# Performance work log

Measured on AMD Instinct MI355X. Metric: run time of the kernel, lower is better.

## Reference

```python
import jax, jax.numpy as jnp
import numpy as np

STOCH, DETER, HID, OBS, ACT = 32, 512, 512, 18, 4
MIN_STD, EPS, UPD_BIAS = 0.1, 1e-3, -1.0


def _ln(x, g, b):
    m = x.mean(-1, keepdims=True)
    v = ((x - m) ** 2).mean(-1, keepdims=True)
    return (x - m) * jax.lax.rsqrt(v + EPS) * g + b


def setup_inputs() -> dict:
    key = jax.random.key(0)
    ks = jax.random.split(key, 10)
    B, T = 256, 256
    def w(k, i, o):
        return jax.random.normal(k, (i, o), jnp.float32) / np.float32(np.sqrt(i))
    return {
        "obs": jax.random.normal(ks[0], (B, T, OBS), jnp.float32),
        "action": jax.random.normal(ks[1], (B, T, ACT), jnp.float32),
        "is_first": jax.random.randint(ks[2], (B, T), 0, 2, jnp.int32),
        "w_prior_in": w(ks[3], STOCH + ACT, HID),
        "g_prior_in": jnp.ones(HID, jnp.float32),
        "bb_prior_in": jnp.zeros(HID, jnp.float32),
        "w_gru": w(ks[4], HID + DETER, 3 * DETER),
        "g_gru": jnp.ones(3 * DETER, jnp.float32),
        "bb_gru": jnp.zeros(3 * DETER, jnp.float32),
        "w_prior_out": w(ks[5], DETER, HID),
        "g_prior_out": jnp.ones(HID, jnp.float32),
        "bb_prior_out": jnp.zeros(HID, jnp.float32),
        "w_prior_stats": w(ks[6], HID, 2 * STOCH),
        "b_prior_stats": jnp.zeros(2 * STOCH, jnp.float32),
        "w_post": w(ks[7], DETER + OBS, HID),
        "g_post": jnp.ones(HID, jnp.float32),
        "bb_post": jnp.zeros(HID, jnp.float32),
        "w_post_stats": w(ks[8], HID, 2 * STOCH),
        "b_post_stats": jnp.zeros(2 * STOCH, jnp.float32),
        "initial_deter": 0.1 * jax.random.normal(ks[9], (1, DETER), jnp.float32),
    }


def reference(obs, action, is_first,
              w_prior_in, g_prior_in, bb_prior_in,
              w_gru, g_gru, bb_gru,
              w_prior_out, g_prior_out, bb_prior_out,
              w_prior_stats, b_prior_stats,
              w_post, g_post, bb_post,
              w_post_stats, b_post_stats,
              initial_deter):
    """RSSM.observe with sample=False. Returns (B, T, 2*(DETER+3*STOCH)):
    concat of post[deter,stoch,mean,std] and prior[deter,stoch,mean,std];
    stoch == mean since dist.mean is used."""
    B = obs.shape[0]
    # learned initial state (identical for every batch row / reset)
    deter0 = jnp.tanh(initial_deter)                                  # (1, DETER)
    h0 = jax.nn.silu(_ln(deter0 @ w_prior_out, g_prior_out, bb_prior_out))
    s0 = h0 @ w_prior_stats + b_prior_stats
    init_mean, _ = jnp.split(s0, 2, axis=-1)                          # (1, STOCH)

    def step(carry, xs):
        deter, stoch = carry
        o_t, a_t, f_t = xs
        mask = (f_t > 0)[:, None]
        deter = jnp.where(mask, deter0, deter)
        stoch = jnp.where(mask, init_mean, stoch)
        a_t = jnp.where(mask, 0.0, a_t)
        # prior_in
        h = jax.nn.silu(_ln(jnp.concatenate([stoch, a_t], -1) @ w_prior_in,
                            g_prior_in, bb_prior_in))
        # GRU cell (depth=1)
        gates = _ln(jnp.concatenate([h, deter], -1) @ w_gru, g_gru, bb_gru)
        r, c, u = jnp.split(gates, 3, axis=-1)
        r = jax.nn.sigmoid(r)
        u = jax.nn.sigmoid(u + UPD_BIAS)
        cand = jax.nn.silu(r * c)
        deter = u * cand + (1.0 - u) * deter
        # prior stats
        h2 = jax.nn.silu(_ln(deter @ w_prior_out, g_prior_out, bb_prior_out))
        ps = h2 @ w_prior_stats + b_prior_stats
        pm, psd = jnp.split(ps, 2, axis=-1)
        psd = jax.nn.softplus(psd) + MIN_STD
        # posterior
        h3 = jax.nn.silu(_ln(jnp.concatenate([deter, o_t], -1) @ w_post,
                             g_post, bb_post))
        qs = h3 @ w_post_stats + b_post_stats
        qm, qsd = jnp.split(qs, 2, axis=-1)
        qsd = jax.nn.softplus(qsd) + MIN_STD
        out = jnp.concatenate([deter, qm, qm, qsd, deter, pm, pm, psd], -1)
        return (deter, qm), out

    carry0 = (jnp.broadcast_to(deter0, (B, DETER)),
              jnp.broadcast_to(init_mean, (B, STOCH)))
    xs = (obs.swapaxes(0, 1), action.swapaxes(0, 1), is_first.swapaxes(0, 1))
    _, ys = jax.lax.scan(step, carry0, xs)   # (T, B, 2*(DETER+3*STOCH))
    return ys.swapaxes(0, 1)
```

## Files before the change

### kernel.cpp

```cpp
#include <hip/hip_runtime.h>

#define TT 256
#define BDIM 256
#define MT 32

typedef unsigned short u16;
typedef unsigned int u32;
typedef __attribute__((ext_vector_type(8))) short bf16x8;
typedef __attribute__((ext_vector_type(4))) float f32x4;

#define GLL(g, l) __builtin_amdgcn_global_load_lds( \
    (const __attribute__((address_space(1))) void*)(g), \
    (__attribute__((address_space(3))) void*)(l), 16, 0, 0)

struct P {
  const float* obs; const float* action; const int* is_first;
  const float* w_prior_in; const float* g_prior_in; const float* bb_prior_in;
  const float* w_gru; const float* g_gru; const float* bb_gru;
  const float* w_prior_out; const float* g_prior_out; const float* bb_prior_out;
  const float* w_prior_stats; const float* b_prior_stats;
  const float* w_post; const float* g_post; const float* bb_post;
  const float* w_post_stats; const float* b_post_stats;
  const float* initial_deter;
  float* out;
  u16 *WgT3;
  u16 *W2T3;
  u16 *WsT3;
  float *deter0, *init_mean;
  int *segb, *segt0, *nact;
  u16 *arow;
  u16 *h2;
  float *gates;
  float *hraw;
  float *deter;
  float *stoch;
  int NB;
};

__device__ __forceinline__ float b2f(u16 u) {
  union { float f; u32 i; } v; v.i = ((u32)u) << 16; return v.f;
}
__device__ __forceinline__ u16 f2b(float f) {
  union { float f; u32 i; } v; v.f = f;
  u32 r = v.i + 0x7FFF + ((v.i >> 16) & 1);
  return (u16)(r >> 16);
}
__device__ __forceinline__ float sigm(float x) { return 1.f / (1.f + __expf(-x)); }
__device__ __forceinline__ float splus(float x) { return x > 15.f ? x : log1pf(__expf(x)); }

__device__ __forceinline__ void awr2(u16* base, int i, int kk, u16 hi, u16 lo) {
  size_t o = (size_t)(kk >> 5) << 11;
  int sw = ((i << 5) + (kk & 31)) ^ ((i & 7) << 3);
  base[o + sw] = hi;
  base[o + 1024 + sw] = lo;
}

__device__ __forceinline__ void h_from_x(const P& p, u16* slotA, int i, float xv, int lane) {
  float a0[8];
  #pragma unroll
  for (int c = 0; c < 8; ++c) a0[c] = 0.f;
  #pragma unroll 4
  for (int j = 0; j < 36; ++j) {
    float s = __shfl(xv, j, 64);
    const float* wr = p.w_prior_in + j * 512 + lane;
    #pragma unroll
    for (int c = 0; c < 8; ++c) a0[c] = fmaf(s, wr[c << 6], a0[c]);
  }
  float sm = 0.f, sq = 0.f;
  #pragma unroll
  for (int c = 0; c < 8; ++c) { sm += a0[c]; sq += a0[c] * a0[c]; }
  #pragma unroll
  for (int o = 32; o; o >>= 1) { sm += __shfl_xor(sm, o); sq += __shfl_xor(sq, o); }
  float m = sm * (1.f / 512.f);
  float rs = rsqrtf(sq * (1.f / 512.f) - m * m + 1e-3f);
  #pragma unroll
  for (int c = 0; c < 8; ++c) {
    int col = lane + (c << 6);
    float v = (a0[c] - m) * rs * p.g_prior_in[col] + p.bb_prior_in[col];
    v = v * sigm(v);
    u16 hi = f2b(v);
    awr2(slotA, i, 544 + col, hi, f2b(v - b2f(hi)));
  }
}

__global__ void k_weights(P p) {
  const int E1 = 192 * 16384, E2 = 68 * 16384, E3 = 32 * 8192;
  const int total = E1 + E2 + E3;
  for (int idx = blockIdx.x * blockDim.x + threadIdx.x; idx < total;
       idx += gridDim.x * blockDim.x) {
    float w; u16* dst;
    int pl;
    if (idx < E1) {
      int kk = idx & 31, prow = (idx >> 5) & 511, img = idx >> 14;
      int pc = img / 6, np = img - pc * 6;
      pl = prow >> 8;
      int n = np * 256 + (prow & 255), k = (pc << 5) + kk;
      w = (k < 512) ? p.w_gru[(512 + k) * 1536 + n] : p.w_gru[(k - 512) * 1536 + n];
      dst = p.WgT3 + ((size_t)img << 14) + (((prow << 5) + kk) ^ ((prow & 7) << 3));
    } else if (idx < E1 + E2) {
      int t = idx - E1;
      int kk = t & 31, prow = (t >> 5) & 511, img = t >> 14;
      int pc = img >> 2, np = img & 3;
      pl = prow >> 8;
      int n = np * 256 + (prow & 255), k = (pc << 5) + kk;
      if (k < 512) w = (n < 512) ? p.w_prior_out[k * 512 + n] : p.w_post[k * 512 + (n - 512)];
      else { int j = k - 512; w = (n >= 512 && j < 18) ? p.w_post[(512 + j) * 512 + (n - 512)] : 0.f; }
      dst = p.W2T3 + ((size_t)img << 14) + (((prow << 5) + kk) ^ ((prow & 7) << 3));
    } else {
      int t = idx - E1 - E2;
      int kk = t & 31, prow = (t >> 5) & 255, pc = t >> 13;
      pl = prow >> 7;
      int nl = prow & 127, k = (pc << 5) + kk;
      if (nl < 64) w = (k < 512) ? p.w_prior_stats[k * 64 + nl] : 0.f;
      else         w = (k >= 512) ? p.w_post_stats[(k - 512) * 64 + (nl - 64)] : 0.f;
      dst = p.WsT3 + ((size_t)pc << 13) + (((prow << 5) + kk) ^ ((prow & 7) << 3));
    }
    u16 hi = f2b(w);
    *dst = pl ? f2b(w - b2f(hi)) : hi;
  }
}

__global__ void k_init_state(P p) {
  __shared__ float d0s[512], tmp[512], red[256];
  int tid = threadIdx.x;
  for (int n = tid; n < 512; n += 256) { d0s[n] = tanhf(p.initial_deter[n]); p.deter0[n] = d0s[n]; }
  __syncthreads();
  for (int n = tid; n < 512; n += 256) {
    float s = 0.f;
    for (int d = 0; d < 512; ++d) s = fmaf(d0s[d], p.w_prior_out[d * 512 + n], s);
    tmp[n] = s;
  }
  __syncthreads();
  float ls = 0.f, lq = 0.f;
  for (int n = tid; n < 512; n += 256) { ls += tmp[n]; lq += tmp[n] * tmp[n]; }
  red[tid] = ls; __syncthreads();
  for (int s = 128; s; s >>= 1) { if (tid < s) red[tid] += red[tid + s]; __syncthreads(); }
  float m = red[0] * (1.f / 512.f); __syncthreads();
  red[tid] = lq; __syncthreads();
  for (int s = 128; s; s >>= 1) { if (tid < s) red[tid] += red[tid + s]; __syncthreads(); }
  float rs = rsqrtf(red[0] * (1.f / 512.f) - m * m + 1e-3f); __syncthreads();
  for (int n = tid; n < 512; n += 256) {
    float h = (tmp[n] - m) * rs * p.g_prior_out[n] + p.bb_prior_out[n];
    tmp[n] = h * sigm(h);
  }
  __syncthreads();
  if (tid < 32) {
    float s = 0.f;
    for (int d = 0; d < 512; ++d) s = fmaf(tmp[d], p.w_prior_stats[d * 64 + tid], s);
    p.init_mean[tid] = s + p.b_prior_stats[tid];
  }
}

__global__ void k_segments(P p) {
  __shared__ int hist[257], off[258], cur[257];
  int tid = threadIdx.x;
  for (int i = tid; i < 257; i += 256) hist[i] = 0;
  __syncthreads();
  int b = tid;
  { int t = 0;
    while (t < TT) {
      int t0 = t; t++;
      while (t < TT && p.is_first[b * TT + t] == 0) t++;
      atomicAdd(&hist[t - t0], 1);
    } }
  __syncthreads();
  if (tid == 0) {
    int run = 0;
    for (int len = 256; len >= 0; --len) { off[len] = run; run += hist[len]; }
  }
  __syncthreads();
  for (int i = tid; i < 257; i += 256) { cur[i] = off[i]; p.nact[i] = off[i]; }
  __syncthreads();
  { int t = 0;
    while (t < TT) {
      int t0 = t; t++;
      while (t < TT && p.is_first[b * TT + t] == 0) t++;
      int idx = atomicAdd(&cur[t - t0], 1);
      p.segb[idx] = b; p.segt0[idx] = t0;
    } }
}

template<int NI, int NSTEPS, int JAT, int RPP>
__device__ __forceinline__ void gemm_pass(
    const u16* __restrict__ aBase, const u16* __restrict__ wBase, int wStride,
    u16* ldsA, u16* ldsW, int wave, int lane, int quad, int l15,
    f32x4 (&acc)[2][NI]) {
  constexpr int GPW = 1 + (RPP >> 5);

  auto stage = [&](int st, int buf) {
    int apc = (st >= JAT) ? st + 1 : st;
    GLL(aBase + ((size_t)apc << 11) + (wave << 9) + (lane << 3),
        ldsA + (buf << 11) + (wave << 9));
    const u16* wS = wBase + (size_t)st * wStride;
    u16* wD = ldsW + (buf << 14);
    #pragma unroll
    for (int pp = 0; pp < 2; ++pp)
      #pragma unroll
      for (int c = 0; c < (RPP >> 6); ++c) {
        int ro = pp * RPP + wave * (RPP >> 2) + (c << 4);
        GLL(wS + (ro << 5) + (lane << 3), wD + (ro << 5));
      }
  };
  auto compute = [&](int buf) {
    const u16* A = ldsA + (buf << 11);
    const u16* W = ldsW + (buf << 14);
    int xr = (l15 & 7) << 3;
    bf16x8 ah[2], al[2];
    #pragma unroll
    for (int mi = 0; mi < 2; ++mi) {
      int r0 = mi * 16 + l15;
      ah[mi] = *(const bf16x8*)&A[((r0 << 5) + (quad << 3)) ^ xr];
      al[mi] = *(const bf16x8*)&A[(((32 + r0) << 5) + (quad << 3)) ^ xr];
    }
    #pragma unroll
    for (int ni = 0; ni < NI; ++ni) {
      int rh = wave * (NI * 16) + ni * 16 + l15;
      bf16x8 wh = *(const bf16x8*)&W[((rh << 5) + (quad << 3)) ^ xr];
      bf16x8 wl = *(const bf16x8*)&W[(((RPP + rh) << 5) + (quad << 3)) ^ xr];
      #pragma unroll
      for (int mi = 0; mi < 2; ++mi) {
        acc[mi][ni] = __builtin_amdgcn_mfma_f32_16x16x32_bf16(ah[mi], wh, acc[mi][ni], 0, 0, 0);
        acc[mi][ni] = __builtin_amdgcn_mfma_f32_16x16x32_bf16(al[mi], wh, acc[mi][ni], 0, 0, 0);
        acc[mi][ni] = __builtin_amdgcn_mfma_f32_16x16x32_bf16(ah[mi], wl, acc[mi][ni], 0, 0, 0);
      }
    }
  };

  stage(0, 0); stage(1, 1); stage(2, 2);
  for (int st = 0; st < NSTEPS; ++st) {
    if (st < NSTEPS - 2)
      asm volatile("s_waitcnt vmcnt(%0)" :: "i"(2 * GPW) : "memory");
    else if (st == NSTEPS - 2)
      asm volatile("s_waitcnt vmcnt(%0)" :: "i"(GPW) : "memory");
    else
      asm volatile("s_waitcnt vmcnt(0)" ::: "memory");
    __builtin_amdgcn_s_barrier();
    __builtin_amdgcn_sched_barrier(0);
    if (st + 3 < NSTEPS) stage(st + 3, (st + 3) & 3);
    compute(st & 3);
  }
}

__global__ void __launch_bounds__(BDIM, 1) k_main(P p) {
  __shared__ u16 lds[73728];
  const int tid = threadIdx.x;
  const int wave = tid >> 6, lane = tid & 63, quad = lane >> 4, l15 = lane & 15;
  u16* ldsA = lds;
  u16* ldsW = lds + 8192;
  const int blk = blockIdx.x;
  u16* slotA = p.arow + (size_t)blk * 67584;
  u16* slotH = p.h2 + (size_t)blk * 65536;
  float* slotG = p.gates + (size_t)blk * 49152;
  float* slotR = p.hraw + (size_t)blk * 32768;
  float* slotD = p.deter + (size_t)blk * 16384;
  float* slotS = p.stoch + (size_t)blk * 1024;
  const int S_total = p.nact[0];
  const int ntiles = (S_total + MT - 1) >> 5;
  const int gmax = (ntiles + 255) & ~255;

  for (int g = blk; g < gmax; g += p.NB) {
    int r = g >> 8, w = g & 255;
    int x = w & 7; if (r & 1) x = 7 - x;
    int t = (r << 8) + (x << 5) + ((w >> 3) & 31);
    if (t >= ntiles) continue;
    int row0 = t << 5;
    int nr0 = S_total - row0; if (nr0 > MT) nr0 = MT;

    for (int k = 0;; ++k) {
      int Mk = p.nact[k] - row0; if (Mk > nr0) Mk = nr0;
      if (Mk <= 0) break;

      for (int i = wave; i < Mk; i += 4) {
        int gi = row0 + i;
        int b = p.segb[gi], t0 = p.segt0[gi];
        float xv = 0.f;
        if (k == 0) {
          #pragma unroll
          for (int c = 0; c < 8; ++c) {
            int d = lane + (c << 6);
            float v = p.deter0[d];
            slotD[i * 512 + d] = v;
            u16 hi = f2b(v);
            awr2(slotA, i, d, hi, f2b(v - b2f(hi)));
          }
          int ff = p.is_first[b * TT + t0];
          if (lane < 32) xv = p.init_mean[lane];
          else if (lane < 36) xv = (ff > 0) ? 0.f : p.action[((size_t)b * TT + t0) * 4 + (lane - 32)];
        } else {
          if (lane < 32) xv = slotS[i * 32 + lane];
          else if (lane < 36) xv = p.action[((size_t)b * TT + t0 + k) * 4 + (lane - 32)];
        }
        h_from_x(p, slotA, i, xv, lane);
      }
      __syncthreads();

      for (int np = 0; np < 6; ++np) {
        __syncthreads();
        f32x4 acc[2][4];
        #pragma unroll
        for (int a = 0; a < 2; ++a)
          #pragma unroll
          for (int bq = 0; bq < 4; ++bq) acc[a][bq] = f32x4{0.f, 0.f, 0.f, 0.f};
        gemm_pass<4, 32, 16, 256>(slotA, p.WgT3 + np * 16384, 98304,
                                  ldsA, ldsW, wave, lane, quad, l15, acc);
        #pragma unroll
        for (int mi = 0; mi < 2; ++mi)
          #pragma unroll
          for (int ni = 0; ni < 4; ++ni)
            #pragma unroll
            for (int rr = 0; rr < 4; ++rr)
              slotG[(mi * 16 + quad * 4 + rr) * 1536 + np * 256 + wave * 64 + ni * 16 + l15]
                  = acc[mi][ni][rr];
      }
      __syncthreads();

      for (int i = wave; i < Mk; i += 4) {
        const float* grow = slotG + i * 1536;
        float g24[24];
        float sm = 0.f, sq = 0.f;
        #pragma unroll
        for (int c = 0; c < 24; ++c) {
          g24[c] = grow[lane + (c << 6)];
          sm += g24[c]; sq += g24[c] * g24[c];
        }
        #pragma unroll
        for (int o = 32; o; o >>= 1) { sm += __shfl_xor(sm, o); sq += __shfl_xor(sq, o); }
        float m = sm * (1.f / 1536.f);
        float rs = rsqrtf(sq * (1.f / 1536.f) - m * m + 1e-3f);
        int gi = row0 + i;
        int b = p.segb[gi], tt = p.segt0[gi] + k;
        float* orow = p.out + ((size_t)b * TT + tt) * 1216;
        #pragma unroll
        for (int c = 0; c < 8; ++c) {
          int d = lane + (c << 6);
          float gr = (g24[c] - m) * rs * p.g_gru[d] + p.bb_gru[d];
          float gc = (g24[c + 8] - m) * rs * p.g_gru[512 + d] + p.bb_gru[512 + d];
          float gu = (g24[c + 16] - m) * rs * p.g_gru[1024 + d] + p.bb_gru[1024 + d];
          float r_ = sigm(gr);
          float u_ = sigm(gu - 1.0f);
          float rc = r_ * gc;
          float cand = rc * sigm(rc);
          float dp = slotD[i * 512 + d];
          float dn = u_ * cand + (1.f - u_) * dp;
          slotD[i * 512 + d] = dn;
          orow[d] = dn; orow[608 + d] = dn;
          u16 hi = f2b(dn);
          awr2(slotA, i, d, hi, f2b(dn - b2f(hi)));
        }
        if (lane < 32) {
          float ov = (lane < 18) ? p.obs[((size_t)b * TT + tt) * 18 + lane] : 0.f;
          u16 hi = f2b(ov);
          awr2(slotA, i, 512 + lane, hi, f2b(ov - b2f(hi)));
        }
      }
      __syncthreads();

      for (int np = 0; np < 4; ++np) {
        __syncthreads();
        f32x4 acc[2][4];
        #pragma unroll
        for (int a = 0; a < 2; ++a)
          #pragma unroll
          for (int bq = 0; bq < 4; ++bq) acc[a][bq] = f32x4{0.f, 0.f, 0.f, 0.f};
        gemm_pass<4, 17, 1000, 256>(slotA, p.W2T3 + np * 16384, 65536,
                                    ldsA, ldsW, wave, lane, quad, l15, acc);
        #pragma unroll
        for (int mi = 0; mi < 2; ++mi)
          #pragma unroll
          for (int ni = 0; ni < 4; ++ni)
            #pragma unroll
            for (int rr = 0; rr < 4; ++rr)
              slotR[(mi * 16 + quad * 4 + rr) * 1024 + np * 256 + wave * 64 + ni * 16 + l15]
                  = acc[mi][ni][rr];
      }
      __syncthreads();

      for (int i = wave; i < Mk; i += 4) {
        #pragma unroll
        for (int hh = 0; hh < 2; ++hh) {
          const float* hb = slotR + i * 1024 + (hh << 9);
          const float* gv = hh ? p.g_post : p.g_prior_out;
          const float* bv = hh ? p.bb_post : p.bb_prior_out;
          float v[8];
          float sm = 0.f, sq = 0.f;
          #pragma unroll
          for (int c = 0; c < 8; ++c) {
            v[c] = hb[lane + (c << 6)];
            sm += v[c]; sq += v[c] * v[c];
          }
          #pragma unroll
          for (int o = 32; o; o >>= 1) { sm += __shfl_xor(sm, o); sq += __shfl_xor(sq, o); }
          float m = sm * (1.f / 512.f);
          float rs = rsqrtf(sq * (1.f / 512.f) - m * m + 1e-3f);
          #pragma unroll
          for (int c = 0; c < 8; ++c) {
            int d = lane + (c << 6);
            float xx = (v[c] - m) * rs * gv[d] + bv[d];
            xx = xx * sigm(xx);
            u16 hi = f2b(xx);
            awr2(slotH, i, (hh << 9) + d, hi, f2b(xx - b2f(hi)));
          }
        }
      }
      __syncthreads();

      {
        f32x4 acc[2][2];
        #pragma unroll
        for (int a = 0; a < 2; ++a)
          #pragma unroll
          for (int bq = 0; bq < 2; ++bq) acc[a][bq] = f32x4{0.f, 0.f, 0.f, 0.f};
        gemm_pass<2, 32, 1000, 128>(slotH, p.WsT3, 8192,
                                    ldsA, ldsW, wave, lane, quad, l15, acc);
        #pragma unroll
        for (int mi = 0; mi < 2; ++mi)
          #pragma unroll
          for (int ni = 0; ni < 2; ++ni)
            #pragma unroll
            for (int rr = 0; rr < 4; ++rr) {
              int i = mi * 16 + quad * 4 + rr;
              int col = wave * 32 + ni * 16 + l15;
              if (i < Mk) {
                float v = acc[mi][ni][rr];
                int gi = row0 + i;
                int b = p.segb[gi], tt = p.segt0[gi] + k;
                float* orow = p.out + ((size_t)b * TT + tt) * 1216;
                if (col < 32) {
                  v += p.b_prior_stats[col];
                  orow[1120 + col] = v; orow[1152 + col] = v;
                } else if (col < 64) {
                  v = splus(v + p.b_prior_stats[col]) + 0.1f;
                  orow[1184 + col - 32] = v;
                } else if (col < 96) {
                  v += p.b_post_stats[col - 64];
                  orow[512 + col - 64] = v; orow[544 + col - 64] = v;
                  slotS[i * 32 + (col - 64)] = v;
                } else {
                  v = splus(v + p.b_post_stats[col - 64]) + 0.1f;
                  orow[576 + col - 96] = v;
                }
              }
            }
      }
      __syncthreads();
    }
  }
}

extern "C" void kernel_launch(void* const* d_in, const int* in_sizes, int n_in,
                              void* d_out, int out_size, void* d_ws, size_t ws_size,
                              hipStream_t stream) {
  P p;
  p.obs = (const float*)d_in[0];
  p.action = (const float*)d_in[1];
  p.is_first = (const int*)d_in[2];
  p.w_prior_in = (const float*)d_in[3];
  p.g_prior_in = (const float*)d_in[4];
  p.bb_prior_in = (const float*)d_in[5];
  p.w_gru = (const float*)d_in[6];
  p.g_gru = (const float*)d_in[7];
  p.bb_gru = (const float*)d_in[8];
  p.w_prior_out = (const float*)d_in[9];
  p.g_prior_out = (const float*)d_in[10];
  p.bb_prior_out = (const float*)d_in[11];
  p.w_prior_stats = (const float*)d_in[12];
  p.b_prior_stats = (const float*)d_in[13];
  p.w_post = (const float*)d_in[14];
  p.g_post = (const float*)d_in[15];
  p.bb_post = (const float*)d_in[16];
  p.w_post_stats = (const float*)d_in[17];
  p.b_post_stats = (const float*)d_in[18];
  p.initial_deter = (const float*)d_in[19];
  p.out = (float*)d_out;

  char* w = (char*)d_ws;
  auto alloc = [&](size_t bytes) -> char* {
    char* r = w; w += (bytes + 255) & ~(size_t)255; return r;
  };
  p.WgT3 = (u16*)alloc((size_t)192 * 16384 * 2);
  p.W2T3 = (u16*)alloc((size_t)68 * 16384 * 2);
  p.WsT3 = (u16*)alloc((size_t)32 * 8192 * 2);
  p.deter0 = (float*)alloc(512 * 4);
  p.init_mean = (float*)alloc(32 * 4);
  p.segb = (int*)alloc((size_t)65536 * 4);
  p.segt0 = (int*)alloc((size_t)65536 * 4);
  p.nact = (int*)alloc(257 * 4);
  size_t used = (size_t)(w - (char*)d_ws);
  size_t avail = ws_size > used ? ws_size - used : 0;
  size_t slot = 666112;
  long long nb = (long long)(avail / slot);
  if (nb > 256) nb = 256;
  if (nb < 1) nb = 1;
  p.NB = (int)nb;
  p.arow = (u16*)alloc((size_t)p.NB * 135168);
  p.h2 = (u16*)alloc((size_t)p.NB * 131072);
  p.gates = (float*)alloc((size_t)p.NB * 196608);
  p.hraw = (float*)alloc((size_t)p.NB * 131072);
  p.deter = (float*)alloc((size_t)p.NB * 65536);
  p.stoch = (float*)alloc((size_t)p.NB * 4096);

  k_weights<<<dim3(256), dim3(256), 0, stream>>>(p);
  k_init_state<<<dim3(1), dim3(256), 0, stream>>>(p);
  k_segments<<<dim3(1), dim3(256), 0, stream>>>(p);
  k_main<<<dim3(p.NB), dim3(BDIM), 0, stream>>>(p);
}
```

Measured before the change: 8.924 ms.

## Keep recurrent state in registers/LDS and stream weights directly into MFMA operands

```diff
diff --git a/kernel.cpp b/kernel.cpp
--- a/kernel.cpp
+++ b/kernel.cpp
@@ -2,7 +2,6 @@
 
 #define TT 256
 #define BDIM 256
-#define MT 32
 
 typedef unsigned short u16;
 typedef unsigned int u32;
@@ -26,14 +25,10 @@
   u16 *WgT3;
   u16 *W2T3;
   u16 *WsT3;
+  float *wpiT;
   float *deter0, *init_mean;
   int *segb, *segt0, *nact;
-  u16 *arow;
   u16 *h2;
-  float *gates;
-  float *hraw;
-  float *deter;
-  float *stoch;
   int NB;
 };
 
@@ -49,22 +44,28 @@
 __device__ __forceinline__ float splus(float x) { return x > 15.f ? x : log1pf(__expf(x)); }
 
 __device__ __forceinline__ void awr2(u16* base, int i, int kk, u16 hi, u16 lo) {
-  size_t o = (size_t)(kk >> 5) << 11;
+  int o = (kk >> 5) << 11;
   int sw = ((i << 5) + (kk & 31)) ^ ((i & 7) << 3);
   base[o + sw] = hi;
   base[o + 1024 + sw] = lo;
 }
 
-__device__ __forceinline__ void h_from_x(const P& p, u16* slotA, int i, float xv, int lane) {
+__device__ __forceinline__ void h_from_x(const P& p, u16* arow, int i, float xv, int lane) {
+  float xs[36];
+  #pragma unroll
+  for (int j = 0; j < 36; ++j) xs[j] = __shfl(xv, j, 64);
   float a0[8];
   #pragma unroll
-  for (int c = 0; c < 8; ++c) a0[c] = 0.f;
-  #pragma unroll 4
-  for (int j = 0; j < 36; ++j) {
-    float s = __shfl(xv, j, 64);
-    const float* wr = p.w_prior_in + j * 512 + lane;
+  for (int c = 0; c < 8; ++c) {
+    const float4* wp = (const float4*)(p.wpiT + (size_t)(lane + (c << 6)) * 36);
+    float s = 0.f;
     #pragma unroll
-    for (int c = 0; c < 8; ++c) a0[c] = fmaf(s, wr[c << 6], a0[c]);
+    for (int t4 = 0; t4 < 9; ++t4) {
+      float4 ww = wp[t4];
+      s = fmaf(xs[4 * t4], ww.x, s); s = fmaf(xs[4 * t4 + 1], ww.y, s);
+      s = fmaf(xs[4 * t4 + 2], ww.z, s); s = fmaf(xs[4 * t4 + 3], ww.w, s);
+    }
+    a0[c] = s;
   }
   float sm = 0.f, sq = 0.f;
   #pragma unroll
@@ -79,44 +80,41 @@
     float v = (a0[c] - m) * rs * p.g_prior_in[col] + p.bb_prior_in[col];
     v = v * sigm(v);
     u16 hi = f2b(v);
-    awr2(slotA, i, 544 + col, hi, f2b(v - b2f(hi)));
+    awr2(arow, i, 544 + col, hi, f2b(v - b2f(hi)));
   }
 }
 
 __global__ void k_weights(P p) {
-  const int E1 = 192 * 16384, E2 = 68 * 16384, E3 = 32 * 8192;
-  const int total = E1 + E2 + E3;
+  const int E1 = 1024 * 1536, E2 = 544 * 1024, E3 = 1024 * 128, E4 = 36 * 512;
+  const int total = E1 + E2 + E3 + E4;
   for (int idx = blockIdx.x * blockDim.x + threadIdx.x; idx < total;
        idx += gridDim.x * blockDim.x) {
-    float w; u16* dst;
-    int pl;
     if (idx < E1) {
-      int kk = idx & 31, prow = (idx >> 5) & 511, img = idx >> 14;
-      int pc = img / 6, np = img - pc * 6;
-      pl = prow >> 8;
-      int n = np * 256 + (prow & 255), k = (pc << 5) + kk;
-      w = (k < 512) ? p.w_gru[(512 + k) * 1536 + n] : p.w_gru[(k - 512) * 1536 + n];
-      dst = p.WgT3 + ((size_t)img << 14) + (((prow << 5) + kk) ^ ((prow & 7) << 3));
+      int k = idx / 1536, n = idx - k * 1536;
+      float w = (k < 512) ? p.w_gru[(512 + k) * 1536 + n] : p.w_gru[(k - 512) * 1536 + n];
+      int np = n >> 8, r = n & 255, pc = k >> 5, kk = k & 31;
+      u16* d = p.WgT3 + ((size_t)(pc * 6 + np) << 14) + (r << 5) + kk;
+      u16 hi = f2b(w); d[0] = hi; d[8192] = f2b(w - b2f(hi));
     } else if (idx < E1 + E2) {
-      int t = idx - E1;
-      int kk = t & 31, prow = (t >> 5) & 511, img = t >> 14;
-      int pc = img >> 2, np = img & 3;
-      pl = prow >> 8;
-      int n = np * 256 + (prow & 255), k = (pc << 5) + kk;
+      int t = idx - E1; int k = t >> 10, n = t & 1023;
+      float w;
       if (k < 512) w = (n < 512) ? p.w_prior_out[k * 512 + n] : p.w_post[k * 512 + (n - 512)];
       else { int j = k - 512; w = (n >= 512 && j < 18) ? p.w_post[(512 + j) * 512 + (n - 512)] : 0.f; }
-      dst = p.W2T3 + ((size_t)img << 14) + (((prow << 5) + kk) ^ ((prow & 7) << 3));
+      int np = n >> 8, r = n & 255, pc = k >> 5, kk = k & 31;
+      u16* d = p.W2T3 + ((size_t)(pc * 4 + np) << 14) + (r << 5) + kk;
+      u16 hi = f2b(w); d[0] = hi; d[8192] = f2b(w - b2f(hi));
+    } else if (idx < E1 + E2 + E3) {
+      int t = idx - E1 - E2; int k = t >> 7, n = t & 127;
+      float w;
+      if (n < 64) w = (k < 512) ? p.w_prior_stats[k * 64 + n] : 0.f;
+      else        w = (k >= 512) ? p.w_post_stats[(k - 512) * 64 + (n - 64)] : 0.f;
+      int pc = k >> 5, kk = k & 31;
+      u16* d = p.WsT3 + ((size_t)pc << 13) + (n << 5) + kk;
+      u16 hi = f2b(w); d[0] = hi; d[4096] = f2b(w - b2f(hi));
     } else {
-      int t = idx - E1 - E2;
-      int kk = t & 31, prow = (t >> 5) & 255, pc = t >> 13;
-      pl = prow >> 7;
-      int nl = prow & 127, k = (pc << 5) + kk;
-      if (nl < 64) w = (k < 512) ? p.w_prior_stats[k * 64 + nl] : 0.f;
-      else         w = (k >= 512) ? p.w_post_stats[(k - 512) * 64 + (nl - 64)] : 0.f;
-      dst = p.WsT3 + ((size_t)pc << 13) + (((prow << 5) + kk) ^ ((prow & 7) << 3));
+      int t = idx - E1 - E2 - E3; int j = t >> 9, col = t & 511;
+      p.wpiT[col * 36 + j] = p.w_prior_in[j * 512 + col];
     }
-    u16 hi = f2b(w);
-    *dst = pl ? f2b(w - b2f(hi)) : hi;
   }
 }
 
@@ -180,96 +178,80 @@
     } }
 }
 
-template<int NI, int NSTEPS, int JAT, int RPP>
-__device__ __forceinline__ void gemm_pass(
-    const u16* __restrict__ aBase, const u16* __restrict__ wBase, int wStride,
-    u16* ldsA, u16* ldsW, int wave, int lane, int quad, int l15,
-    f32x4 (&acc)[2][NI]) {
-  constexpr int GPW = 1 + (RPP >> 5);
-
-  auto stage = [&](int st, int buf) {
-    int apc = (st >= JAT) ? st + 1 : st;
-    GLL(aBase + ((size_t)apc << 11) + (wave << 9) + (lane << 3),
-        ldsA + (buf << 11) + (wave << 9));
-    const u16* wS = wBase + (size_t)st * wStride;
-    u16* wD = ldsW + (buf << 14);
+template<int NSTEPS, int JAT>
+__device__ __forceinline__ void gemm_nb(
+    const u16* aLds, const u16* wImg, size_t wStride,
+    int wave, int quad, int l15, int xr, f32x4 (&acc)[2][4]) {
+  const u16* wq = wImg + ((((wave << 6) + l15) << 5) + (quad << 3));
+  bf16x8 H0[4], L0[4], H1[4], L1[4], H2[4], L2[4];
+  auto ld = [&](bf16x8 (&H)[4], bf16x8 (&L)[4]) {
     #pragma unroll
-    for (int pp = 0; pp < 2; ++pp)
-      #pragma unroll
-      for (int c = 0; c < (RPP >> 6); ++c) {
-        int ro = pp * RPP + wave * (RPP >> 2) + (c << 4);
-        GLL(wS + (ro << 5) + (lane << 3), wD + (ro << 5));
-      }
+    for (int ni = 0; ni < 4; ++ni) {
+      H[ni] = *(const bf16x8*)(wq + (ni << 9));
+      L[ni] = *(const bf16x8*)(wq + 8192 + (ni << 9));
+    }
+    wq += wStride;
   };
-  auto compute = [&](int buf) {
-    const u16* A = ldsA + (buf << 11);
-    const u16* W = ldsW + (buf << 14);
-    int xr = (l15 & 7) << 3;
+  auto cp = [&](int st, bf16x8 (&H)[4], bf16x8 (&L)[4]) {
+    int apc = st + (st >= JAT ? 1 : 0);
+    const u16* A = aLds + (apc << 11);
     bf16x8 ah[2], al[2];
     #pragma unroll
     for (int mi = 0; mi < 2; ++mi) {
-      int r0 = mi * 16 + l15;
-      ah[mi] = *(const bf16x8*)&A[((r0 << 5) + (quad << 3)) ^ xr];
-      al[mi] = *(const bf16x8*)&A[(((32 + r0) << 5) + (quad << 3)) ^ xr];
+      int off = ((((mi << 4) + l15) << 5) + (quad << 3)) ^ xr;
+      ah[mi] = *(const bf16x8*)&A[off];
+      al[mi] = *(const bf16x8*)&A[off + 1024];
     }
     #pragma unroll
-    for (int ni = 0; ni < NI; ++ni) {
-      int rh = wave * (NI * 16) + ni * 16 + l15;
-      bf16x8 wh = *(const bf16x8*)&W[((rh << 5) + (quad << 3)) ^ xr];
-      bf16x8 wl = *(const bf16x8*)&W[(((RPP + rh) << 5) + (quad << 3)) ^ xr];
+    for (int ni = 0; ni < 4; ++ni)
       #pragma unroll
       for (int mi = 0; mi < 2; ++mi) {
-        acc[mi][ni] = __builtin_amdgcn_mfma_f32_16x16x32_bf16(ah[mi], wh, acc[mi][ni], 0, 0, 0);
-        acc[mi][ni] = __builtin_amdgcn_mfma_f32_16x16x32_bf16(al[mi], wh, acc[mi][ni], 0, 0, 0);
-        acc[mi][ni] = __builtin_amdgcn_mfma_f32_16x16x32_bf16(ah[mi], wl, acc[mi][ni], 0, 0, 0);
+        acc[mi][ni] = __builtin_amdgcn_mfma_f32_16x16x32_bf16(ah[mi], H[ni], acc[mi][ni], 0, 0, 0);
+        acc[mi][ni] = __builtin_amdgcn_mfma_f32_16x16x32_bf16(al[mi], H[ni], acc[mi][ni], 0, 0, 0);
+        acc[mi][ni] = __builtin_amdgcn_mfma_f32_16x16x32_bf16(ah[mi], L[ni], acc[mi][ni], 0, 0, 0);
       }
-    }
   };
-
-  stage(0, 0); stage(1, 1); stage(2, 2);
-  for (int st = 0; st < NSTEPS; ++st) {
-    if (st < NSTEPS - 2)
-      asm volatile("s_waitcnt vmcnt(%0)" :: "i"(2 * GPW) : "memory");
-    else if (st == NSTEPS - 2)
-      asm volatile("s_waitcnt vmcnt(%0)" :: "i"(GPW) : "memory");
-    else
-      asm volatile("s_waitcnt vmcnt(0)" ::: "memory");
-    __builtin_amdgcn_s_barrier();
-    __builtin_amdgcn_sched_barrier(0);
-    if (st + 3 < NSTEPS) stage(st + 3, (st + 3) & 3);
-    compute(st & 3);
-  }
+  static_assert(NSTEPS % 3 == 2, "tail assumes NSTEPS==2 mod 3");
+  ld(H0, L0); ld(H1, L1);
+  for (int st = 0; st + 2 < NSTEPS; st += 3) {
+    ld(H2, L2); cp(st, H0, L0);
+    ld(H0, L0); cp(st + 1, H1, L1);
+    ld(H1, L1); cp(st + 2, H2, L2);
+  }
+  cp(NSTEPS - 2, H0, L0);
+  cp(NSTEPS - 1, H1, L1);
 }
 
 __global__ void __launch_bounds__(BDIM, 1) k_main(P p) {
   __shared__ u16 lds[73728];
+  __shared__ float lnscr[4][32][4];
+  __shared__ float stochs[1024];
+  __shared__ int orowt[32];
   const int tid = threadIdx.x;
   const int wave = tid >> 6, lane = tid & 63, quad = lane >> 4, l15 = lane & 15;
-  u16* ldsA = lds;
-  u16* ldsW = lds + 8192;
+  const int xr = (l15 & 7) << 3;
+  u16* arow = lds;
+  u16* fb = lds + 67584;
   const int blk = blockIdx.x;
-  u16* slotA = p.arow + (size_t)blk * 67584;
   u16* slotH = p.h2 + (size_t)blk * 65536;
-  float* slotG = p.gates + (size_t)blk * 49152;
-  float* slotR = p.hraw + (size_t)blk * 32768;
-  float* slotD = p.deter + (size_t)blk * 16384;
-  float* slotS = p.stoch + (size_t)blk * 1024;
   const int S_total = p.nact[0];
-  const int ntiles = (S_total + MT - 1) >> 5;
+  const int ntiles = (S_total + 31) >> 5;
   const int gmax = (ntiles + 255) & ~255;
 
   for (int g = blk; g < gmax; g += p.NB) {
-    int r = g >> 8, w = g & 255;
-    int x = w & 7; if (r & 1) x = 7 - x;
-    int t = (r << 8) + (x << 5) + ((w >> 3) & 31);
+    int rr_ = g >> 8, w = g & 255;
+    int x = w & 7; if (rr_ & 1) x = 7 - x;
+    int t = (rr_ << 8) + (x << 5) + ((w >> 3) & 31);
     if (t >= ntiles) continue;
     int row0 = t << 5;
-    int nr0 = S_total - row0; if (nr0 > MT) nr0 = MT;
+    int nr0 = S_total - row0; if (nr0 > 32) nr0 = 32;
 
     for (int k = 0;; ++k) {
       int Mk = p.nact[k] - row0; if (Mk > nr0) Mk = nr0;
       if (Mk <= 0) break;
 
+      if (tid < 32)
+        orowt[tid] = (tid < Mk) ? (p.segb[row0 + tid] * TT + p.segt0[row0 + tid] + k) : -1;
       for (int i = wave; i < Mk; i += 4) {
         int gi = row0 + i;
         int b = p.segb[gi], t0 = p.segt0[gi];
@@ -279,152 +261,284 @@
           for (int c = 0; c < 8; ++c) {
             int d = lane + (c << 6);
             float v = p.deter0[d];
-            slotD[i * 512 + d] = v;
             u16 hi = f2b(v);
-            awr2(slotA, i, d, hi, f2b(v - b2f(hi)));
+            awr2(arow, i, d, hi, f2b(v - b2f(hi)));
           }
           int ff = p.is_first[b * TT + t0];
           if (lane < 32) xv = p.init_mean[lane];
           else if (lane < 36) xv = (ff > 0) ? 0.f : p.action[((size_t)b * TT + t0) * 4 + (lane - 32)];
         } else {
-          if (lane < 32) xv = slotS[i * 32 + lane];
+          if (lane < 32) xv = stochs[(i << 5) + lane];
           else if (lane < 36) xv = p.action[((size_t)b * TT + t0 + k) * 4 + (lane - 32)];
         }
-        h_from_x(p, slotA, i, xv, lane);
+        int tc = t0 + k;
+        if (lane < 32) {
+          float ov = (lane < 18) ? p.obs[((size_t)b * TT + tc) * 18 + lane] : 0.f;
+          u16 hi = f2b(ov);
+          awr2(arow, i, 512 + lane, hi, f2b(ov - b2f(hi)));
+        }
+        h_from_x(p, arow, i, xv, lane);
       }
       __syncthreads();
 
+      f32x4 acc[6][2][4];
+      #pragma unroll
       for (int np = 0; np < 6; ++np) {
-        __syncthreads();
-        f32x4 acc[2][4];
-        #pragma unroll
-        for (int a = 0; a < 2; ++a)
-          #pragma unroll
-          for (int bq = 0; bq < 4; ++bq) acc[a][bq] = f32x4{0.f, 0.f, 0.f, 0.f};
-        gemm_pass<4, 32, 16, 256>(slotA, p.WgT3 + np * 16384, 98304,
-                                  ldsA, ldsW, wave, lane, quad, l15, acc);
-        #pragma unroll
-        for (int mi = 0; mi < 2; ++mi)
-          #pragma unroll
-          for (int ni = 0; ni < 4; ++ni)
-            #pragma unroll
-            for (int rr = 0; rr < 4; ++rr)
-              slotG[(mi * 16 + quad * 4 + rr) * 1536 + np * 256 + wave * 64 + ni * 16 + l15]
-                  = acc[mi][ni][rr];
+        #pragma unroll
+        for (int mi = 0; mi < 2; ++mi)
+          #pragma unroll
+          for (int ni = 0; ni < 4; ++ni) acc[np][mi][ni] = f32x4{0.f, 0.f, 0.f, 0.f};
+        gemm_nb<32, 16>(arow, p.WgT3 + np * 16384, (size_t)6 * 16384,
+                        wave, quad, l15, xr, acc[np]);
       }
       __syncthreads();
 
-      for (int i = wave; i < Mk; i += 4) {
-        const float* grow = slotG + i * 1536;
-        float g24[24];
-        float sm = 0.f, sq = 0.f;
-        #pragma unroll
-        for (int c = 0; c < 24; ++c) {
-          g24[c] = grow[lane + (c << 6)];
-          sm += g24[c]; sq += g24[c] * g24[c];
+      {
+        float smv[2][4], sqv[2][4];
+        #pragma unroll
+        for (int mi = 0; mi < 2; ++mi)
+          #pragma unroll
+          for (int rg = 0; rg < 4; ++rg) { smv[mi][rg] = 0.f; sqv[mi][rg] = 0.f; }
+        #pragma unroll
+        for (int np = 0; np < 6; ++np)
+          #pragma unroll
+          for (int mi = 0; mi < 2; ++mi)
+            #pragma unroll
+            for (int ni = 0; ni < 4; ++ni)
+              #pragma unroll
+              for (int rg = 0; rg < 4; ++rg) {
+                float v = acc[np][mi][ni][rg];
+                smv[mi][rg] += v; sqv[mi][rg] += v * v;
+              }
+        #pragma unroll
+        for (int mi = 0; mi < 2; ++mi)
+          #pragma unroll
+          for (int rg = 0; rg < 4; ++rg) {
+            float s = smv[mi][rg], qv = sqv[mi][rg];
+            #pragma unroll
+            for (int o = 1; o < 16; o <<= 1) { s += __shfl_xor(s, o); qv += __shfl_xor(qv, o); }
+            smv[mi][rg] = s; sqv[mi][rg] = qv;
+          }
+        if (l15 == 0) {
+          #pragma unroll
+          for (int mi = 0; mi < 2; ++mi)
+            #pragma unroll
+            for (int rg = 0; rg < 4; ++rg) {
+              int row = (mi << 4) + (quad << 2) + rg;
+              lnscr[wave][row][0] = smv[mi][rg];
+              lnscr[wave][row][1] = sqv[mi][rg];
+            }
         }
-        #pragma unroll
-        for (int o = 32; o; o >>= 1) { sm += __shfl_xor(sm, o); sq += __shfl_xor(sq, o); }
-        float m = sm * (1.f / 1536.f);
-        float rs = rsqrtf(sq * (1.f / 1536.f) - m * m + 1e-3f);
-        int gi = row0 + i;
-        int b = p.segb[gi], tt = p.segt0[gi] + k;
-        float* orow = p.out + ((size_t)b * TT + tt) * 1216;
-        #pragma unroll
-        for (int c = 0; c < 8; ++c) {
-          int d = lane + (c << 6);
-          float gr = (g24[c] - m) * rs * p.g_gru[d] + p.bb_gru[d];
-          float gc = (g24[c + 8] - m) * rs * p.g_gru[512 + d] + p.bb_gru[512 + d];
-          float gu = (g24[c + 16] - m) * rs * p.g_gru[1024 + d] + p.bb_gru[1024 + d];
-          float r_ = sigm(gr);
-          float u_ = sigm(gu - 1.0f);
-          float rc = r_ * gc;
-          float cand = rc * sigm(rc);
-          float dp = slotD[i * 512 + d];
-          float dn = u_ * cand + (1.f - u_) * dp;
-          slotD[i * 512 + d] = dn;
-          orow[d] = dn; orow[608 + d] = dn;
-          u16 hi = f2b(dn);
-          awr2(slotA, i, d, hi, f2b(dn - b2f(hi)));
+        __syncthreads();
+        #pragma unroll
+        for (int mi = 0; mi < 2; ++mi)
+          #pragma unroll
+          for (int rg = 0; rg < 4; ++rg) {
+            int row = (mi << 4) + (quad << 2) + rg;
+            float a0 = 0.f, a1 = 0.f;
+            #pragma unroll
+            for (int w2 = 0; w2 < 4; ++w2) {
+              a0 += lnscr[w2][row][0]; a1 += lnscr[w2][row][1];
+            }
+            float m_ = a0 * (1.f / 1536.f);
+            smv[mi][rg] = m_;
+            sqv[mi][rg] = rsqrtf(a1 * (1.f / 1536.f) - m_ * m_ + 1e-3f);
+          }
+        #pragma unroll
+        for (int hh = 0; hh < 2; ++hh)
+          #pragma unroll
+          for (int ni = 0; ni < 4; ++ni) {
+            int dcol = (hh << 8) + (wave << 6) + (ni << 4) + l15;
+            float gR = p.g_gru[dcol], gC = p.g_gru[512 + dcol], gU = p.g_gru[1024 + dcol];
+            float bR = p.bb_gru[dcol], bC = p.bb_gru[512 + dcol], bU = p.bb_gru[1024 + dcol];
+            int pcD = dcol >> 5, kkD = dcol & 31;
+            #pragma unroll
+            for (int mi = 0; mi < 2; ++mi)
+              #pragma unroll
+              for (int rg = 0; rg < 4; ++rg) {
+                int row = (mi << 4) + (quad << 2) + rg;
+                float m_ = smv[mi][rg], rs_ = sqv[mi][rg];
+                float vr = (acc[hh][mi][ni][rg] - m_) * rs_ * gR + bR;
+                float vc = (acc[2 + hh][mi][ni][rg] - m_) * rs_ * gC + bC;
+                float vu = (acc[4 + hh][mi][ni][rg] - m_) * rs_ * gU + bU;
+                float r_ = sigm(vr), u_ = sigm(vu - 1.f);
+                float rc = r_ * vc, cand = rc * sigm(rc);
+                int ab = (pcD << 11) + (((row << 5) + kkD) ^ ((row & 7) << 3));
+                float dp = b2f(arow[ab]) + b2f(arow[ab + 1024]);
+                float dn = u_ * cand + (1.f - u_) * dp;
+                u16 hi = f2b(dn);
+                arow[ab] = hi; arow[ab + 1024] = f2b(dn - b2f(hi));
+                int ot = orowt[row];
+                if (ot >= 0) {
+                  float* orow = p.out + (size_t)ot * 1216;
+                  orow[dcol] = dn; orow[608 + dcol] = dn;
+                }
+              }
+          }
+      }
+      __syncthreads();
+
+      f32x4 dac[4][2][4];
+      #pragma unroll
+      for (int np = 0; np < 4; ++np) {
+        #pragma unroll
+        for (int mi = 0; mi < 2; ++mi)
+          #pragma unroll
+          for (int ni = 0; ni < 4; ++ni) dac[np][mi][ni] = f32x4{0.f, 0.f, 0.f, 0.f};
+        gemm_nb<17, 100>(arow, p.W2T3 + np * 16384, (size_t)4 * 16384,
+                         wave, quad, l15, xr, dac[np]);
+      }
+      {
+        float sP[2][4], qP[2][4], sQ[2][4], qQ[2][4];
+        #pragma unroll
+        for (int mi = 0; mi < 2; ++mi)
+          #pragma unroll
+          for (int rg = 0; rg < 4; ++rg) { sP[mi][rg]=0.f; qP[mi][rg]=0.f; sQ[mi][rg]=0.f; qQ[mi][rg]=0.f; }
+        #pragma unroll
+        for (int np = 0; np < 4; ++np)
+          #pragma unroll
+          for (int mi = 0; mi < 2; ++mi)
+            #pragma unroll
+            for (int ni = 0; ni < 4; ++ni)
+              #pragma unroll
+              for (int rg = 0; rg < 4; ++rg) {
+                float v = dac[np][mi][ni][rg];
+                if (np < 2) { sP[mi][rg] += v; qP[mi][rg] += v * v; }
+                else        { sQ[mi][rg] += v; qQ[mi][rg] += v * v; }
+              }
+        #pragma unroll
+        for (int mi = 0; mi < 2; ++mi)
+          #pragma unroll
+          for (int rg = 0; rg < 4; ++rg) {
+            float a0 = sP[mi][rg], a1 = qP[mi][rg], a2 = sQ[mi][rg], a3 = qQ[mi][rg];
+            #pragma unroll
+            for (int o = 1; o < 16; o <<= 1) {
+              a0 += __shfl_xor(a0, o); a1 += __shfl_xor(a1, o);
+              a2 += __shfl_xor(a2, o); a3 += __shfl_xor(a3, o);
+            }
+            sP[mi][rg] = a0; qP[mi][rg] = a1; sQ[mi][rg] = a2; qQ[mi][rg] = a3;
+          }
+        if (l15 == 0) {
+          #pragma unroll
+          for (int mi = 0; mi < 2; ++mi)
+            #pragma unroll
+            for (int rg = 0; rg < 4; ++rg) {
+              int row = (mi << 4) + (quad << 2) + rg;
+              lnscr[wave][row][0] = sP[mi][rg]; lnscr[wave][row][1] = qP[mi][rg];
+              lnscr[wave][row][2] = sQ[mi][rg]; lnscr[wave][row][3] = qQ[mi][rg];
+            }
         }
-        if (lane < 32) {
-          float ov = (lane < 18) ? p.obs[((size_t)b * TT + tt) * 18 + lane] : 0.f;
-          u16 hi = f2b(ov);
-          awr2(slotA, i, 512 + lane, hi, f2b(ov - b2f(hi)));
+        __syncthreads();
+        float mP[2][4], rP[2][4], mQ[2][4], rQ[2][4];
+        #pragma unroll
+        for (int mi = 0; mi < 2; ++mi)
+          #pragma unroll
+          for (int rg = 0; rg < 4; ++rg) {
+            int row = (mi << 4) + (quad << 2) + rg;
+            float a0 = 0.f, a1 = 0.f, a2 = 0.f, a3 = 0.f;
+            #pragma unroll
+            for (int w2 = 0; w2 < 4; ++w2) {
+              a0 += lnscr[w2][row][0]; a1 += lnscr[w2][row][1];
+              a2 += lnscr[w2][row][2]; a3 += lnscr[w2][row][3];
+            }
+            mP[mi][rg] = a0 * (1.f / 512.f);
+            rP[mi][rg] = rsqrtf(a1 * (1.f / 512.f) - mP[mi][rg] * mP[mi][rg] + 1e-3f);
+            mQ[mi][rg] = a2 * (1.f / 512.f);
+            rQ[mi][rg] = rsqrtf(a3 * (1.f / 512.f) - mQ[mi][rg] * mQ[mi][rg] + 1e-3f);
+          }
+        #pragma unroll
+        for (int np = 0; np < 4; ++np) {
+          const int half = np >> 1;
+          #pragma unroll
+          for (int ni = 0; ni < 4; ++ni) {
+            int col = (np << 8) + (wave << 6) + (ni << 4) + l15;
+            int c5 = col & 511;
+            float gv = half ? p.g_post[c5] : p.g_prior_out[c5];
+            float bv = half ? p.bb_post[c5] : p.bb_prior_out[c5];
+            int pcH = col >> 5, kkH = col & 31;
+            #pragma unroll
+            for (int mi = 0; mi < 2; ++mi)
+              #pragma unroll
+              for (int rg = 0; rg < 4; ++rg) {
+                int row = (mi << 4) + (quad << 2) + rg;
+                float m_ = half ? mQ[mi][rg] : mP[mi][rg];
+                float rs_ = half ? rQ[mi][rg] : rP[mi][rg];
+                float xx = (dac[np][mi][ni][rg] - m_) * rs_ * gv + bv;
+                xx = xx * sigm(xx);
+                u16 hi = f2b(xx);
+                size_t e = ((size_t)pcH << 11) + (((row << 5) + kkH) ^ ((row & 7) << 3));
+                slotH[e] = hi; slotH[e + 1024] = f2b(xx - b2f(hi));
+              }
+          }
         }
       }
       __syncthreads();
 
-      for (int np = 0; np < 4; ++np) {
-        __syncthreads();
-        f32x4 acc[2][4];
-        #pragma unroll
-        for (int a = 0; a < 2; ++a)
-          #pragma unroll
-          for (int bq = 0; bq < 4; ++bq) acc[a][bq] = f32x4{0.f, 0.f, 0.f, 0.f};
-        gemm_pass<4, 17, 1000, 256>(slotA, p.W2T3 + np * 16384, 65536,
-                                    ldsA, ldsW, wave, lane, quad, l15, acc);
-        #pragma unroll
-        for (int mi = 0; mi < 2; ++mi)
-          #pragma unroll
-          for (int ni = 0; ni < 4; ++ni)
-            #pragma unroll
-            for (int rr = 0; rr < 4; ++rr)
-              slotR[(mi * 16 + quad * 4 + rr) * 1024 + np * 256 + wave * 64 + ni * 16 + l15]
-                  = acc[mi][ni][rr];
-      }
-      __syncthreads();
-
-      for (int i = wave; i < Mk; i += 4) {
-        #pragma unroll
-        for (int hh = 0; hh < 2; ++hh) {
-          const float* hb = slotR + i * 1024 + (hh << 9);
-          const float* gv = hh ? p.g_post : p.g_prior_out;
-          const float* bv = hh ? p.bb_post : p.bb_prior_out;
-          float v[8];
-          float sm = 0.f, sq = 0.f;
-          #pragma unroll
-          for (int c = 0; c < 8; ++c) {
-            v[c] = hb[lane + (c << 6)];
-            sm += v[c]; sq += v[c] * v[c];
-          }
-          #pragma unroll
-          for (int o = 32; o; o >>= 1) { sm += __shfl_xor(sm, o); sq += __shfl_xor(sq, o); }
-          float m = sm * (1.f / 512.f);
-          float rs = rsqrtf(sq * (1.f / 512.f) - m * m + 1e-3f);
-          #pragma unroll
-          for (int c = 0; c < 8; ++c) {
-            int d = lane + (c << 6);
-            float xx = (v[c] - m) * rs * gv[d] + bv[d];
-            xx = xx * sigm(xx);
-            u16 hi = f2b(xx);
-            awr2(slotH, i, (hh << 9) + d, hi, f2b(xx - b2f(hi)));
-          }
+      {
+        const u16* wq0 = p.WsT3 + (((wave << 5) + l15) << 5) + (quad << 3);
+        f32x4 fac[2][2];
+        #pragma unroll
+        for (int mi = 0; mi < 2; ++mi)
+          #pragma unroll
+          for (int ni = 0; ni < 2; ++ni) fac[mi][ni] = f32x4{0.f, 0.f, 0.f, 0.f};
+        bf16x8 FH0[2], FL0[2], FH1[2], FL1[2];
+        auto stF = [&](int st, int buf) {
+          GLL(slotH + (st << 11) + (wave << 9) + (lane << 3),
+              fb + (buf << 11) + (wave << 9));
+        };
+        auto ldF = [&](int st, bf16x8 (&FH)[2], bf16x8 (&FL)[2]) {
+          const u16* qq = wq0 + ((size_t)st << 13);
+          #pragma unroll
+          for (int ni = 0; ni < 2; ++ni) {
+            FH[ni] = *(const bf16x8*)(qq + (ni << 9));
+            FL[ni] = *(const bf16x8*)(qq + 4096 + (ni << 9));
+          }
+        };
+        auto cpF = [&](int st, bf16x8 (&FH)[2], bf16x8 (&FL)[2]) {
+          const u16* A = fb + ((st % 3) << 11);
+          bf16x8 ah[2], al[2];
+          #pragma unroll
+          for (int mi = 0; mi < 2; ++mi) {
+            int off = ((((mi << 4) + l15) << 5) + (quad << 3)) ^ xr;
+            ah[mi] = *(const bf16x8*)&A[off];
+            al[mi] = *(const bf16x8*)&A[off + 1024];
+          }
+          #pragma unroll
+          for (int ni = 0; ni < 2; ++ni)
+            #pragma unroll
+            for (int mi = 0; mi < 2; ++mi) {
+              fac[mi][ni] = __builtin_amdgcn_mfma_f32_16x16x32_bf16(ah[mi], FH[ni], fac[mi][ni], 0, 0, 0);
+              fac[mi][ni] = __builtin_amdgcn_mfma_f32_16x16x32_bf16(al[mi], FH[ni], fac[mi][ni], 0, 0, 0);
+              fac[mi][ni] = __builtin_amdgcn_mfma_f32_16x16x32_bf16(ah[mi], FL[ni], fac[mi][ni], 0, 0, 0);
+            }
+        };
+        stF(0, 0); stF(1, 1); ldF(0, FH0, FL0);
+        for (int st = 0; st < 32; st += 2) {
+          asm volatile("s_waitcnt vmcnt(5)" ::: "memory");
+          __builtin_amdgcn_s_barrier();
+          __builtin_amdgcn_sched_barrier(0);
+          if (st + 2 < 32) stF(st + 2, (st + 2) % 3);
+          ldF(st + 1, FH1, FL1);
+          cpF(st, FH0, FL0);
+          asm volatile("s_waitcnt vmcnt(5)" ::: "memory");
+          __builtin_amdgcn_s_barrier();
+          __builtin_amdgcn_sched_barrier(0);
+          if (st + 3 < 32) stF(st + 3, (st + 3) % 3);
+          if (st + 2 < 32) ldF(st + 2, FH0, FL0);
+          cpF(st + 1, FH1, FL1);
         }
-      }
-      __syncthreads();
-
-      {
-        f32x4 acc[2][2];
-        #pragma unroll
-        for (int a = 0; a < 2; ++a)
-          #pragma unroll
-          for (int bq = 0; bq < 2; ++bq) acc[a][bq] = f32x4{0.f, 0.f, 0.f, 0.f};
-        gemm_pass<2, 32, 1000, 128>(slotH, p.WsT3, 8192,
-                                    ldsA, ldsW, wave, lane, quad, l15, acc);
         #pragma unroll
         for (int mi = 0; mi < 2; ++mi)
           #pragma unroll
           for (int ni = 0; ni < 2; ++ni)
             #pragma unroll
-            for (int rr = 0; rr < 4; ++rr) {
-              int i = mi * 16 + quad * 4 + rr;
-              int col = wave * 32 + ni * 16 + l15;
+            for (int rg = 0; rg < 4; ++rg) {
+              int i = (mi << 4) + (quad << 2) + rg;
+              int col = (wave << 5) + (ni << 4) + l15;
               if (i < Mk) {
-                float v = acc[mi][ni][rr];
-                int gi = row0 + i;
-                int b = p.segb[gi], tt = p.segt0[gi] + k;
-                float* orow = p.out + ((size_t)b * TT + tt) * 1216;
+                float v = fac[mi][ni][rg];
+                int ot = orowt[i];
+                float* orow = p.out + (size_t)ot * 1216;
                 if (col < 32) {
                   v += p.b_prior_stats[col];
                   orow[1120 + col] = v; orow[1152 + col] = v;
@@ -434,7 +548,7 @@
                 } else if (col < 96) {
                   v += p.b_post_stats[col - 64];
                   orow[512 + col - 64] = v; orow[544 + col - 64] = v;
-                  slotS[i * 32 + (col - 64)] = v;
+                  stochs[(i << 5) + (col - 64)] = v;
                 } else {
                   v = splus(v + p.b_post_stats[col - 64]) + 0.1f;
                   orow[576 + col - 96] = v;
@@ -480,6 +594,7 @@
   p.WgT3 = (u16*)alloc((size_t)192 * 16384 * 2);
   p.W2T3 = (u16*)alloc((size_t)68 * 16384 * 2);
   p.WsT3 = (u16*)alloc((size_t)32 * 8192 * 2);
+  p.wpiT = (float*)alloc((size_t)512 * 36 * 4);
   p.deter0 = (float*)alloc(512 * 4);
   p.init_mean = (float*)alloc(32 * 4);
   p.segb = (int*)alloc((size_t)65536 * 4);
@@ -487,17 +602,11 @@
   p.nact = (int*)alloc(257 * 4);
   size_t used = (size_t)(w - (char*)d_ws);
   size_t avail = ws_size > used ? ws_size - used : 0;
-  size_t slot = 666112;
-  long long nb = (long long)(avail / slot);
+  long long nb = (long long)(avail / 131072);
   if (nb > 256) nb = 256;
   if (nb < 1) nb = 1;
   p.NB = (int)nb;
-  p.arow = (u16*)alloc((size_t)p.NB * 135168);
   p.h2 = (u16*)alloc((size_t)p.NB * 131072);
-  p.gates = (float*)alloc((size_t)p.NB * 196608);
-  p.hraw = (float*)alloc((size_t)p.NB * 131072);
-  p.deter = (float*)alloc((size_t)p.NB * 65536);
-  p.stoch = (float*)alloc((size_t)p.NB * 4096);
 
   k_weights<<<dim3(256), dim3(256), 0, stream>>>(p);
   k_init_state<<<dim3(1), dim3(256), 0, stream>>>(p);
```

After: 9.857 ms. +10.5%, slower.
